# Kernel tuning notes

Measured on AMD Instinct MI355X. Metric: run time of the kernel, lower is better.

The kernel has to match this reference:

```python
import jax, jax.numpy as jnp
import numpy as np

GROUP_SIZE = 64  # quantization group size along in_features (K)


def setup_inputs() -> dict:
    key = jax.random.key(0)
    k1, k2, k3, k4, k5 = jax.random.split(key, 5)
    M, K, N = 32, 8192, 8192
    num_groups = K // GROUP_SIZE
    x = jax.random.normal(k1, (M, K), dtype=jnp.float32)
    # packed int4 weights: two nibbles per byte along K -> [N, K//2]
    packed_weight = jax.random.randint(k2, (N, K // 2), 0, 256, dtype=jnp.int32)
    scales = jax.random.uniform(k3, (N, num_groups), dtype=jnp.float32) * 0.02 + 1e-3
    zeros = jax.random.uniform(k4, (N, num_groups), dtype=jnp.float32) * 15.0
    bias_param = jax.random.normal(k5, (N,), dtype=jnp.float32)
    return {"x": x, "packed_weight": packed_weight, "scales": scales,
            "zeros": zeros, "bias_param": bias_param}


def reference(x, packed_weight, scales, zeros, bias_param):
    # x: [M, K] float; packed_weight: [N, K//2] int (uint8 semantics)
    # scales/zeros: [N, num_groups]; bias_param: [N]
    K = x.shape[-1]
    k = jnp.arange(K)
    shift = (k % 2) * 4                     # low nibble for even k, high for odd
    # unpack int4: q[n, k] in [0, 15]
    q = (packed_weight[:, k // 2] >> shift[None, :]) & 15   # [N, K]
    gidx = k // GROUP_SIZE                                  # [K]
    # group-wise dequant: (q - zero) * scale
    w = (q.astype(jnp.float32) - zeros[:, gidx]) * scales[:, gidx]  # [N, K]
    out = jnp.einsum('mk,nk->mn', x, w) + bias_param[None, :]        # [M, N]
    return out
```

## Files before the change

kernel.cpp:

```cpp
#include <hip/hip_runtime.h>
#include <hip/hip_bf16.h>
#include <stdint.h>


#define KK 8192
#define NN 8192
#define KP 4096
#define NG 128
#define BN 16
#define KSPLIT 2
#define KSW 32
#define NKS 256
#define NCH 16
#define BUFB 6144
#define WREG (3 * BUFB)

typedef __attribute__((ext_vector_type(8))) short short8;
typedef __attribute__((ext_vector_type(4))) float floatx4;
typedef const __attribute__((address_space(1))) void* gbl_t;
typedef __attribute__((address_space(3))) void* lds_t;

__device__ __forceinline__ void async16(const void* g, void* l) {
    __builtin_amdgcn_global_load_lds((gbl_t)(uintptr_t)g, (lds_t)(uintptr_t)l, 16, 0, 0);
}

__device__ __forceinline__ unsigned pack_bf16x2(float lo, float hi) {
    union { __hip_bfloat162 h; unsigned u; } c;
    c.h = __float22bfloat162_rn(make_float2(lo, hi));
    return c.u;
}

__device__ __forceinline__ unsigned dq2(int q, float sc, float zs) {
    float lo = fmaf((float)(q & 15),        sc, zs);
    float hi = fmaf((float)((q >> 4) & 15), sc, zs);
    unsigned ua = __float_as_uint(lo); ua += 0x7fffu + ((ua >> 16) & 1u);
    unsigned ub = __float_as_uint(hi); ub += 0x7fffu + ((ub >> 16) & 1u);
    return __builtin_amdgcn_perm(ub, ua, 0x07060302);
}

__global__ void prep_kernel(const float* __restrict__ x, const float* __restrict__ bias,
                            ushort* __restrict__ xb, float* __restrict__ out,
                            int xconv_blocks)
{
    const int bx = blockIdx.x;
    if (bx < xconv_blocks) {
        const int tid = bx * 256 + threadIdx.x;
        const int l   = tid & 63;
        const int ks  = (tid >> 6) & 255;
        const int mt  = tid >> 14;
        const int m   = (l & 15) + 16 * mt;
        const int kb  = ks * 32 + (l >> 4) * 8;
        const float* src = x + (size_t)m * KK + kb;
        const float4 a = *(const float4*)(src);
        const float4 b = *(const float4*)(src + 4);
        *(uint4*)(xb + (size_t)tid * 8) =
            make_uint4(pack_bf16x2(a.x, a.y), pack_bf16x2(a.z, a.w),
                       pack_bf16x2(b.x, b.y), pack_bf16x2(b.z, b.w));
    } else {
        const int f4 = (bx - xconv_blocks) * 256 + threadIdx.x;
        const int n4 = f4 & (NN / 4 - 1);
        ((float4*)out)[f4] = ((const float4*)bias)[n4];
    }
}

__global__ __launch_bounds__(256, 2)
void gptq_mfma_lds(const int*   __restrict__ pw,
                   const float* __restrict__ scales,
                   const float* __restrict__ zeros,
                   const ushort* __restrict__ xb,
                   float* __restrict__ out)
{
    __shared__ uint4 smem4[4 * WREG / 16];
    uint8_t* smem = (uint8_t*)smem4;

    const int tid  = threadIdx.x;
    const int lane = tid & 63;
    const int wave = tid >> 6;
    const int kh   = blockIdx.x & (KSPLIT - 1);
    const int n0   = (blockIdx.x >> 1) * BN;
    const int nl   = lane & 15;
    const int kq   = lane >> 4;
    const int ks0  = kh * 128 + wave * KSW;
    const int g0   = ks0 >> 1;

    float scr[16], zsr[16];
    {
        const float* sp = scales + (size_t)(n0 + nl) * NG + g0;
        const float* zp = zeros  + (size_t)(n0 + nl) * NG + g0;
#pragma unroll
        for (int i = 0; i < 4; ++i) {
            const float4 s4 = *(const float4*)(sp + i * 4);
            const float4 z4 = *(const float4*)(zp + i * 4);
            scr[i*4+0] = s4.x; zsr[i*4+0] = -z4.x * s4.x;
            scr[i*4+1] = s4.y; zsr[i*4+1] = -z4.y * s4.y;
            scr[i*4+2] = s4.z; zsr[i*4+2] = -z4.z * s4.z;
            scr[i*4+3] = s4.w; zsr[i*4+3] = -z4.w * s4.w;
        }
    }

    const int srow = lane >> 3;
    const int st   = lane & 7;
    const int swz  = st ^ srow;
    const int* pg0 = pw + (size_t)(n0 + 0 + srow) * KP + ks0 * 16 + swz * 4;
    const int* pg1 = pw + (size_t)(n0 + 8 + srow) * KP + ks0 * 16 + swz * 4;
    const uint4* xg0 = (const uint4*)xb + (size_t)(0 * NKS + ks0) * 64 + lane;
    const uint4* xg1 = (const uint4*)xb + (size_t)(1 * NKS + ks0) * 64 + lane;

    uint8_t* wbase = smem + wave * WREG;

#define STAGE(c) do {                                        \
        uint8_t* b_ = wbase + ((c) % 3) * BUFB;              \
        async16(pg0 + (c) * 32, b_);                         \
        async16(pg1 + (c) * 32, b_ + 1024);                  \
        async16(xg0 + (c) * 128,      b_ + 2048);            \
        async16(xg0 + (c) * 128 + 64, b_ + 3072);            \
        async16(xg1 + (c) * 128,      b_ + 4096);            \
        async16(xg1 + (c) * 128 + 64, b_ + 5120);            \
    } while (0)

    const int pwo0 = nl * 128 + (((0 * 4 + kq) ^ (nl & 7)) * 16);
    const int pwo1 = nl * 128 + (((1 * 4 + kq) ^ (nl & 7)) * 16);
    const int xo   = lane * 16;

    floatx4 acc0 = {0.f, 0.f, 0.f, 0.f};
    floatx4 acc1 = {0.f, 0.f, 0.f, 0.f};

    STAGE(0);
    STAGE(1);

#pragma unroll
    for (int c = 0; c < NCH; ++c) {
        if (c + 2 < NCH) {
            STAGE(c + 2);
            asm volatile("s_waitcnt vmcnt(12)" ::: "memory");
        } else if (c == NCH - 2) {
            asm volatile("s_waitcnt vmcnt(6)" ::: "memory");
        } else {
            asm volatile("s_waitcnt vmcnt(0)" ::: "memory");
        }
        uint8_t* b = wbase + (c % 3) * BUFB;
        const float sc = scr[c];
        const float zs = zsr[c];
#pragma unroll
        for (int j = 0; j < 2; ++j) {
            const int4  p  = *(const int4*) (b + (j ? pwo1 : pwo0));
            union { uint4 v; short8 s; } a0, a1, bf;
            a0.v = *(const uint4*)(b + 2048 + j * 1024 + xo);
            a1.v = *(const uint4*)(b + 4096 + j * 1024 + xo);
            bf.v.x = dq2(p.x, sc, zs);
            bf.v.y = dq2(p.y, sc, zs);
            bf.v.z = dq2(p.z, sc, zs);
            bf.v.w = dq2(p.w, sc, zs);
            acc0 = __builtin_amdgcn_mfma_f32_16x16x32_bf16(a0.s, bf.s, acc0, 0, 0, 0);
            acc1 = __builtin_amdgcn_mfma_f32_16x16x32_bf16(a1.s, bf.s, acc1, 0, 0, 0);
        }
    }
#undef STAGE

    __syncthreads();
    float* red = (float*)smem;
#pragma unroll
    for (int r = 0; r < 4; ++r) {
        const int row = kq * 4 + r;
        red[(wave * 2 + 0) * 256 + row * 16 + nl] = acc0[r];
        red[(wave * 2 + 1) * 256 + row * 16 + nl] = acc1[r];
    }
    __syncthreads();

#pragma unroll
    for (int i = 0; i < 2; ++i) {
        const int e   = i * 256 + tid;
        const int mt  = e >> 8;
        const int idx = e & 255;
        const float s = red[(0 * 2 + mt) * 256 + idx] + red[(1 * 2 + mt) * 256 + idx]
                      + red[(2 * 2 + mt) * 256 + idx] + red[(3 * 2 + mt) * 256 + idx];
        atomicAdd(out + (size_t)(mt * 16 + (idx >> 4)) * NN + n0 + (idx & 15), s);
    }
}

__global__ __launch_bounds__(256, 4)
void gptq_mfma_fallback(const int*   __restrict__ pw,
                        const float* __restrict__ scales,
                        const float* __restrict__ zeros,
                        const float* __restrict__ x,
                        float* __restrict__ out)
{
    __shared__ float s_lds[64][BN + 1];
    __shared__ float z_lds[64][BN + 1];
    __shared__ float red[4][2][256];

    const int tid  = threadIdx.x;
    const int lane = tid & 63;
    const int wave = tid >> 6;
    const int kh   = blockIdx.x & (KSPLIT - 1);
    const int n0   = (blockIdx.x >> 1) * BN;
    const int g0   = kh * 64;

    {
        const int r  = tid >> 4;
        const int gb = (tid & 15) * 4;
        const float4 s4 = *(const float4*)(scales + (size_t)(n0 + r) * NG + g0 + gb);
        const float4 z4 = *(const float4*)(zeros  + (size_t)(n0 + r) * NG + g0 + gb);
        s_lds[gb + 0][r] = s4.x; s_lds[gb + 1][r] = s4.y;
        s_lds[gb + 2][r] = s4.z; s_lds[gb + 3][r] = s4.w;
        z_lds[gb + 0][r] = z4.x; z_lds[gb + 1][r] = z4.y;
        z_lds[gb + 2][r] = z4.z; z_lds[gb + 3][r] = z4.w;
    }
    __syncthreads();

    const int nl = lane & 15;
    const int kq = lane >> 4;
    const int* pwp = pw + (size_t)(n0 + nl) * KP + kq * 4;
    const int ks0 = kh * 128 + wave * KSW;

    auto load_xfrag = [&](int mt, int ks) -> uint4 {
        const float* src = x + (size_t)(nl + 16 * mt) * KK + ks * 32 + kq * 8;
        const float4 a = *(const float4*)(src);
        const float4 b = *(const float4*)(src + 4);
        return make_uint4(pack_bf16x2(a.x, a.y), pack_bf16x2(a.z, a.w),
                          pack_bf16x2(b.x, b.y), pack_bf16x2(b.z, b.w));
    };

    floatx4 acc0 = {0.f, 0.f, 0.f, 0.f};
    floatx4 acc1 = {0.f, 0.f, 0.f, 0.f};
    int4  pwb[4];
    uint4 x0b[4], x1b[4];

#pragma unroll
    for (int i = 0; i < 3; ++i) {
        const int ks = ks0 + i;
        pwb[i] = *(const int4*)(pwp + ks * 16);
        x0b[i] = load_xfrag(0, ks);
        x1b[i] = load_xfrag(1, ks);
    }

#pragma unroll 4
    for (int i = 0; i < KSW; ++i) {
        const int slot = i & 3;
        if (i + 3 < KSW) {
            const int ks = ks0 + i + 3;
            const int ps = (i + 3) & 3;
            pwb[ps] = *(const int4*)(pwp + ks * 16);
            x0b[ps] = load_xfrag(0, ks);
            x1b[ps] = load_xfrag(1, ks);
        }
        const int gl  = (wave * KSW + i) >> 1;
        const float sc = s_lds[gl][nl];
        const float zs = -z_lds[gl][nl] * sc;

        union { uint4 v; short8 s; } bf, a0, a1;
        const int4 p = pwb[slot];
        bf.v.x = dq2(p.x, sc, zs);
        bf.v.y = dq2(p.y, sc, zs);
        bf.v.z = dq2(p.z, sc, zs);
        bf.v.w = dq2(p.w, sc, zs);
        a0.v = x0b[slot];
        a1.v = x1b[slot];
        acc0 = __builtin_amdgcn_mfma_f32_16x16x32_bf16(a0.s, bf.s, acc0, 0, 0, 0);
        acc1 = __builtin_amdgcn_mfma_f32_16x16x32_bf16(a1.s, bf.s, acc1, 0, 0, 0);
    }

#pragma unroll
    for (int r = 0; r < 4; ++r) {
        const int row = kq * 4 + r;
        red[wave][0][row * 16 + nl] = acc0[r];
        red[wave][1][row * 16 + nl] = acc1[r];
    }
    __syncthreads();

#pragma unroll
    for (int i = 0; i < 2; ++i) {
        const int e   = i * 256 + tid;
        const int mt  = e >> 8;
        const int idx = e & 255;
        const float s = red[0][mt][idx] + red[1][mt][idx] + red[2][mt][idx] + red[3][mt][idx];
        atomicAdd(out + (size_t)(mt * 16 + (idx >> 4)) * NN + n0 + (idx & 15), s);
    }
}

extern "C" void kernel_launch(void* const* d_in, const int* in_sizes, int n_in,
                              void* d_out, int out_size, void* d_ws, size_t ws_size,
                              hipStream_t stream) {
    const float* x      = (const float*)d_in[0];
    const int*   pw     = (const int*)  d_in[1];
    const float* scales = (const float*)d_in[2];
    const float* zeros  = (const float*)d_in[3];
    const float* bias   = (const float*)d_in[4];
    float* out = (float*)d_out;

    const size_t need = (size_t)32768 * 16;
    if (d_ws != nullptr && ws_size >= need) {
        ushort* xb = (ushort*)d_ws;
        prep_kernel<<<128 + 256, 256, 0, stream>>>(x, bias, xb, out, 128);
        gptq_mfma_lds<<<512 * KSPLIT, 256, 0, stream>>>(pw, scales, zeros, xb, out);
    } else {
        prep_kernel<<<256, 256, 0, stream>>>(x, bias, nullptr, out, 0);
        gptq_mfma_fallback<<<512 * KSPLIT, 256, 0, stream>>>(pw, scales, zeros, x, out);
    }
}
```

Measured before the change: 210.8 us.

## Drop K-split and atomics, stream weights via LDS, read activations directly from global

Removes the 2-way K split so each block covers the full K range for 16 output columns. The final reduction now writes output plus bias directly instead of using atomics, and the prep kernel no longer initialises the output with bias. Only packed weights are staged into LDS (double-buffered, 8 async loads per stage, new swizzle). Activation fragments are loaded straight from global memory, where they are expected to hit in cache. This gives half as many blocks (512, each twice as long) and increases per-wave register use for scales and zeros, in exchange for less atomic traffic and a lighter prep kernel.

```diff
diff --git a/kernel.cpp b/kernel.cpp
--- a/kernel.cpp
+++ b/kernel.cpp
@@ -8,12 +8,12 @@
 #define KP 4096
 #define NG 128
 #define BN 16
+#define KSW 64
+#define NKS 256
+#define SCK 8
+#define NSC 8
+#define PWBUF 8192
 #define KSPLIT 2
-#define KSW 32
-#define NKS 256
-#define NCH 16
-#define BUFB 6144
-#define WREG (3 * BUFB)
 
 typedef __attribute__((ext_vector_type(8))) short short8;
 typedef __attribute__((ext_vector_type(4))) float floatx4;
@@ -64,31 +64,30 @@
 }
 
 __global__ __launch_bounds__(256, 2)
-void gptq_mfma_lds(const int*   __restrict__ pw,
-                   const float* __restrict__ scales,
-                   const float* __restrict__ zeros,
-                   const ushort* __restrict__ xb,
-                   float* __restrict__ out)
+void gptq_mfma_main(const int*   __restrict__ pw,
+                    const float* __restrict__ scales,
+                    const float* __restrict__ zeros,
+                    const float* __restrict__ bias,
+                    const ushort* __restrict__ xb,
+                    float* __restrict__ out)
 {
-    __shared__ uint4 smem4[4 * WREG / 16];
+    __shared__ uint4 smem4[65536 / 16];
     uint8_t* smem = (uint8_t*)smem4;
 
     const int tid  = threadIdx.x;
     const int lane = tid & 63;
     const int wave = tid >> 6;
-    const int kh   = blockIdx.x & (KSPLIT - 1);
-    const int n0   = (blockIdx.x >> 1) * BN;
+    const int n0   = blockIdx.x * BN;
     const int nl   = lane & 15;
     const int kq   = lane >> 4;
-    const int ks0  = kh * 128 + wave * KSW;
-    const int g0   = ks0 >> 1;
-
-    float scr[16], zsr[16];
+    const int ks0  = wave * KSW;
+
+    float scr[32], zsr[32];
     {
-        const float* sp = scales + (size_t)(n0 + nl) * NG + g0;
-        const float* zp = zeros  + (size_t)(n0 + nl) * NG + g0;
-#pragma unroll
-        for (int i = 0; i < 4; ++i) {
+        const float* sp = scales + (size_t)(n0 + nl) * NG + wave * 32;
+        const float* zp = zeros  + (size_t)(n0 + nl) * NG + wave * 32;
+#pragma unroll
+        for (int i = 0; i < 8; ++i) {
             const float4 s4 = *(const float4*)(sp + i * 4);
             const float4 z4 = *(const float4*)(zp + i * 4);
             scr[i*4+0] = s4.x; zsr[i*4+0] = -z4.x * s4.x;
@@ -98,61 +97,57 @@
         }
     }
 
-    const int srow = lane >> 3;
-    const int st   = lane & 7;
-    const int swz  = st ^ srow;
-    const int* pg0 = pw + (size_t)(n0 + 0 + srow) * KP + ks0 * 16 + swz * 4;
-    const int* pg1 = pw + (size_t)(n0 + 8 + srow) * KP + ks0 * 16 + swz * 4;
-    const uint4* xg0 = (const uint4*)xb + (size_t)(0 * NKS + ks0) * 64 + lane;
-    const uint4* xg1 = (const uint4*)xb + (size_t)(1 * NKS + ks0) * 64 + lane;
-
-    uint8_t* wbase = smem + wave * WREG;
-
-#define STAGE(c) do {                                        \
-        uint8_t* b_ = wbase + ((c) % 3) * BUFB;              \
-        async16(pg0 + (c) * 32, b_);                         \
-        async16(pg1 + (c) * 32, b_ + 1024);                  \
-        async16(xg0 + (c) * 128,      b_ + 2048);            \
-        async16(xg0 + (c) * 128 + 64, b_ + 3072);            \
-        async16(xg1 + (c) * 128,      b_ + 4096);            \
-        async16(xg1 + (c) * 128 + 64, b_ + 5120);            \
+    const int hw = lane >> 5, h = lane & 31, js = h >> 2, q = h & 3;
+    int bofs[8];
+#pragma unroll
+    for (int i = 0; i < 8; ++i) {
+        const int r  = 2 * i + hw;
+        const int jg = js ^ (r & 7);
+        const int qg = q ^ (i & 3);
+        bofs[i] = (n0 + r) * KP + jg * 16 + qg * 4;
+    }
+    uint8_t* wbuf = smem + wave * (2 * PWBUF);
+    const int pwo = (nl >> 1) * 1024 + (nl & 1) * 512 + ((kq ^ ((nl >> 1) & 3)) * 16);
+    const int jx  = nl & 7;
+
+#define STAGE(s) do {                                                  \
+        uint8_t* b_ = wbuf + ((s) & 1) * PWBUF;                        \
+        const int kb16_ = (ks0 + (s) * SCK) * 16;                      \
+        _Pragma("unroll")                                              \
+        for (int i_ = 0; i_ < 8; ++i_)                                 \
+            async16(pw + bofs[i_] + kb16_, b_ + i_ * 1024);            \
     } while (0)
 
-    const int pwo0 = nl * 128 + (((0 * 4 + kq) ^ (nl & 7)) * 16);
-    const int pwo1 = nl * 128 + (((1 * 4 + kq) ^ (nl & 7)) * 16);
-    const int xo   = lane * 16;
-
+    const uint4* xfp = (const uint4*)xb;
     floatx4 acc0 = {0.f, 0.f, 0.f, 0.f};
     floatx4 acc1 = {0.f, 0.f, 0.f, 0.f};
 
     STAGE(0);
-    STAGE(1);
-
-#pragma unroll
-    for (int c = 0; c < NCH; ++c) {
-        if (c + 2 < NCH) {
-            STAGE(c + 2);
-            asm volatile("s_waitcnt vmcnt(12)" ::: "memory");
-        } else if (c == NCH - 2) {
-            asm volatile("s_waitcnt vmcnt(6)" ::: "memory");
+
+#pragma unroll
+    for (int s = 0; s < NSC; ++s) {
+        if (s + 1 < NSC) {
+            STAGE(s + 1);
+            asm volatile("s_waitcnt vmcnt(8)" ::: "memory");
         } else {
             asm volatile("s_waitcnt vmcnt(0)" ::: "memory");
         }
-        uint8_t* b = wbase + (c % 3) * BUFB;
-        const float sc = scr[c];
-        const float zs = zsr[c];
-#pragma unroll
-        for (int j = 0; j < 2; ++j) {
-            const int4  p  = *(const int4*) (b + (j ? pwo1 : pwo0));
-            union { uint4 v; short8 s; } a0, a1, bf;
-            a0.v = *(const uint4*)(b + 2048 + j * 1024 + xo);
-            a1.v = *(const uint4*)(b + 4096 + j * 1024 + xo);
+        uint8_t* b = wbuf + (s & 1) * PWBUF;
+#pragma unroll
+        for (int j = 0; j < SCK; ++j) {
+            const int ks = ks0 + s * SCK + j;
+            const int4 p = *(const int4*)(b + pwo + ((j ^ jx) * 64));
+            union { uint4 v; short8 sv; } a0, a1, bf;
+            a0.v = xfp[(size_t)(0 * NKS + ks) * 64 + lane];
+            a1.v = xfp[(size_t)(1 * NKS + ks) * 64 + lane];
+            const float sc = scr[s * 4 + (j >> 1)];
+            const float zs = zsr[s * 4 + (j >> 1)];
             bf.v.x = dq2(p.x, sc, zs);
             bf.v.y = dq2(p.y, sc, zs);
             bf.v.z = dq2(p.z, sc, zs);
             bf.v.w = dq2(p.w, sc, zs);
-            acc0 = __builtin_amdgcn_mfma_f32_16x16x32_bf16(a0.s, bf.s, acc0, 0, 0, 0);
-            acc1 = __builtin_amdgcn_mfma_f32_16x16x32_bf16(a1.s, bf.s, acc1, 0, 0, 0);
+            acc0 = __builtin_amdgcn_mfma_f32_16x16x32_bf16(a0.sv, bf.sv, acc0, 0, 0, 0);
+            acc1 = __builtin_amdgcn_mfma_f32_16x16x32_bf16(a1.sv, bf.sv, acc1, 0, 0, 0);
         }
     }
 #undef STAGE
@@ -172,9 +167,10 @@
         const int e   = i * 256 + tid;
         const int mt  = e >> 8;
         const int idx = e & 255;
-        const float s = red[(0 * 2 + mt) * 256 + idx] + red[(1 * 2 + mt) * 256 + idx]
-                      + red[(2 * 2 + mt) * 256 + idx] + red[(3 * 2 + mt) * 256 + idx];
-        atomicAdd(out + (size_t)(mt * 16 + (idx >> 4)) * NN + n0 + (idx & 15), s);
+        const float sv = red[(0 * 2 + mt) * 256 + idx] + red[(1 * 2 + mt) * 256 + idx]
+                       + red[(2 * 2 + mt) * 256 + idx] + red[(3 * 2 + mt) * 256 + idx];
+        const int n = n0 + (idx & 15);
+        out[(size_t)(mt * 16 + (idx >> 4)) * NN + n] = sv + bias[n];
     }
 }
 
@@ -211,7 +207,7 @@
     const int nl = lane & 15;
     const int kq = lane >> 4;
     const int* pwp = pw + (size_t)(n0 + nl) * KP + kq * 4;
-    const int ks0 = kh * 128 + wave * KSW;
+    const int ks0 = kh * 128 + wave * 32;
 
     auto load_xfrag = [&](int mt, int ks) -> uint4 {
         const float* src = x + (size_t)(nl + 16 * mt) * KK + ks * 32 + kq * 8;
@@ -235,20 +231,20 @@
     }
 
 #pragma unroll 4
-    for (int i = 0; i < KSW; ++i) {
+    for (int i = 0; i < 32; ++i) {
         const int slot = i & 3;
-        if (i + 3 < KSW) {
+        if (i + 3 < 32) {
             const int ks = ks0 + i + 3;
             const int ps = (i + 3) & 3;
             pwb[ps] = *(const int4*)(pwp + ks * 16);
             x0b[ps] = load_xfrag(0, ks);
             x1b[ps] = load_xfrag(1, ks);
         }
-        const int gl  = (wave * KSW + i) >> 1;
+        const int gl  = (wave * 32 + i) >> 1;
         const float sc = s_lds[gl][nl];
         const float zs = -z_lds[gl][nl] * sc;
 
-        union { uint4 v; short8 s; } bf, a0, a1;
+        union { uint4 v; short8 sv; } bf, a0, a1;
         const int4 p = pwb[slot];
         bf.v.x = dq2(p.x, sc, zs);
         bf.v.y = dq2(p.y, sc, zs);
@@ -256,8 +252,8 @@
         bf.v.w = dq2(p.w, sc, zs);
         a0.v = x0b[slot];
         a1.v = x1b[slot];
-        acc0 = __builtin_amdgcn_mfma_f32_16x16x32_bf16(a0.s, bf.s, acc0, 0, 0, 0);
-        acc1 = __builtin_amdgcn_mfma_f32_16x16x32_bf16(a1.s, bf.s, acc1, 0, 0, 0);
+        acc0 = __builtin_amdgcn_mfma_f32_16x16x32_bf16(a0.sv, bf.sv, acc0, 0, 0, 0);
+        acc1 = __builtin_amdgcn_mfma_f32_16x16x32_bf16(a1.sv, bf.sv, acc1, 0, 0, 0);
     }
 
 #pragma unroll
@@ -291,8 +287,8 @@
     const size_t need = (size_t)32768 * 16;
     if (d_ws != nullptr && ws_size >= need) {
         ushort* xb = (ushort*)d_ws;
-        prep_kernel<<<128 + 256, 256, 0, stream>>>(x, bias, xb, out, 128);
-        gptq_mfma_lds<<<512 * KSPLIT, 256, 0, stream>>>(pw, scales, zeros, xb, out);
+        prep_kernel<<<128, 256, 0, stream>>>(x, bias, xb, out, 128);
+        gptq_mfma_main<<<NN / BN, 256, 0, stream>>>(pw, scales, zeros, bias, xb, out);
     } else {
         prep_kernel<<<256, 256, 0, stream>>>(x, bias, nullptr, out, 0);
         gptq_mfma_fallback<<<512 * KSPLIT, 256, 0, stream>>>(pw, scales, zeros, x, out);
```

After: 209.9 us. No clear change (-0.4%).
